# Kernel tuning notes

Measured on AMD Instinct MI355X. Metric: run time of the kernel, lower is better.

The kernel has to match this reference:

```python
import jax, jax.numpy as jnp
import numpy as np

N = 50000      # nodes
E = 600000     # edges
G = 256        # graphs in batch
HID = 128      # gcn hidden = gcn in = gcn out
EDIM = 16      # edge feature dim
EH = 64        # edge mlp hidden
NL = 4         # gcn layers
MIN_ = 200     # mol feature dim
MH = 256       # mlp hidden
MOUT = 128     # mlp out
PH = 512       # predictor hidden
PIN = HID + MOUT


def setup_inputs() -> dict:
    key = jax.random.key(0)
    ks = jax.random.split(key, 32)
    f = lambda k, s: jax.random.normal(k, s, dtype=jnp.float32)
    p = lambda k, s: 0.05 * jax.random.normal(k, s, dtype=jnp.float32)
    return {
        "x": f(ks[0], (N, HID)),
        "edge_index": jax.random.randint(ks[1], (2, E), 0, N),
        "edge_attr": f(ks[2], (E, EDIM)),
        "batch_index": jnp.sort(jax.random.randint(ks[3], (N,), 0, G)),
        "mol_features": f(ks[4], (G, MIN_)),
        # PDNConv params (stacked over NL layers)
        "conv_lin_W": p(ks[5], (NL, HID, HID)),
        "conv_mW1": p(ks[6], (NL, EDIM, EH)),
        "conv_mb1": p(ks[7], (NL, EH)),
        "conv_mW2": p(ks[8], (NL, EH)),
        "conv_mb2": p(ks[9], (NL,)),
        "conv_bias": p(ks[10], (NL, HID)),
        # dense Linear after each conv
        "gcn_W": p(ks[11], (NL, HID, HID)),
        "gcn_b": p(ks[12], (NL, HID)),
        # mol-feature MLP (n_mlp_layers=3 -> 4 linears)
        "mlp_W0": p(ks[13], (MIN_, MH)), "mlp_b0": p(ks[14], (MH,)),
        "mlp_W1": p(ks[15], (MH, MH)),   "mlp_b1": p(ks[16], (MH,)),
        "mlp_W2": p(ks[17], (MH, MH)),   "mlp_b2": p(ks[18], (MH,)),
        "mlp_W3": p(ks[19], (MH, MOUT)), "mlp_b3": p(ks[20], (MOUT,)),
        # predictor
        "pred_W0": p(ks[21], (PIN, PH)), "pred_b0": p(ks[22], (PH,)),
        "pred_W1": p(ks[23], (PH, PH)),  "pred_b1": p(ks[24], (PH,)),
        "out_W": p(ks[25], (PH, 1)),     "out_b": p(ks[26], (1,)),
    }


def _pdn_conv(h, row, col, edge_attr, lin_W, mW1, mb1, mW2, mb2, bias):
    # edge MLP -> sigmoid gate (PyG PDNConv)
    w = jax.nn.sigmoid(jnp.maximum(edge_attr @ mW1 + mb1, 0.0) @ mW2 + mb2)  # [E]
    # gcn_norm with self loops (fill weight 1.0)
    loop = jnp.arange(N)
    r = jnp.concatenate([row, loop])
    c = jnp.concatenate([col, loop])
    w_all = jnp.concatenate([w, jnp.ones((N,), h.dtype)])
    deg = jax.ops.segment_sum(w_all, c, num_segments=N)
    dinv = jnp.where(deg > 0, jax.lax.rsqrt(deg), 0.0)
    norm = dinv[r] * w_all * dinv[c]                                          # [E+N]
    hl = h @ lin_W                                                            # [N,HID]
    out = jax.ops.segment_sum(norm[:, None] * hl[r], c, num_segments=N)
    return out + bias


def reference(x, edge_index, edge_attr, batch_index, mol_features,
              conv_lin_W, conv_mW1, conv_mb1, conv_mW2, conv_mb2, conv_bias,
              gcn_W, gcn_b,
              mlp_W0, mlp_b0, mlp_W1, mlp_b1, mlp_W2, mlp_b2, mlp_W3, mlp_b3,
              pred_W0, pred_b0, pred_W1, pred_b1, out_W, out_b):
    row, col = edge_index[0], edge_index[1]
    relu = lambda v: jnp.maximum(v, 0.0)

    # GCN stack: PDNConv -> relu(Linear), x NL
    h1 = x
    for i in range(NL):
        h1 = _pdn_conv(h1, row, col, edge_attr, conv_lin_W[i], conv_mW1[i],
                       conv_mb1[i], conv_mW2[i], conv_mb2[i], conv_bias[i])
        h1 = relu(h1 @ gcn_W[i] + gcn_b[i])
    # global mean pool over graphs
    sums = jax.ops.segment_sum(h1, batch_index, num_segments=G)
    cnts = jax.ops.segment_sum(jnp.ones((N,), h1.dtype), batch_index, num_segments=G)
    h1 = sums / jnp.maximum(cnts, 1.0)[:, None]                               # [G,HID]

    # molecular-feature MLP
    h2 = relu(mol_features @ mlp_W0 + mlp_b0)
    h2 = relu(h2 @ mlp_W1 + mlp_b1)
    h2 = relu(h2 @ mlp_W2 + mlp_b2)
    h2 = relu(h2 @ mlp_W3 + mlp_b3)                                           # [G,MOUT]

    h = jnp.concatenate([h1, h2], axis=1)                                     # [G,PIN]
    h = relu(h @ pred_W0 + pred_b0)
    h = relu(h @ pred_W1 + pred_b1)
    return h @ out_W + out_b                                                  # [G,1]
```

## Files before the change

kernel.cpp:

```cpp
#include <hip/hip_runtime.h>
#include <hip/hip_bf16.h>


#define NN 50000
#define EE 600000
#define GG 256
#define HID 128
#define EDIM 16
#define EHID 64
#define NL 4
#define MIN_F 200
#define MH 256
#define MOUT 128
#define PH 512
#define PIN 256
#define SCAN_B 196
#define PCH 8

typedef __hip_bfloat16 bf16;
typedef __attribute__((ext_vector_type(8))) short bf16x8;
typedef __attribute__((ext_vector_type(4))) float f32x4;

__device__ __forceinline__ float bfl(unsigned u) { return __uint_as_float(u << 16); }
__device__ __forceinline__ float bfh(unsigned u) { return __uint_as_float(u & 0xffff0000u); }
__device__ __forceinline__ float b2f(bf16 x) { return __bfloat162float(x); }
__device__ __forceinline__ float ldf(const void* p, long i, bool bf) {
  return bf ? __bfloat162float(((const bf16*)p)[i]) : ((const float*)p)[i];
}
__device__ __forceinline__ unsigned short f2bf_bits(float v) {
  bf16 h = __float2bfloat16(v);
  return *reinterpret_cast<unsigned short*>(&h);
}

__global__ void probe_kernel(const unsigned short* __restrict__ xs, int* flag) {
  if (threadIdx.x == 0 && blockIdx.x == 0) {
    int sane = 0;
    for (int i = 0; i < 128; i++) {
      unsigned e = (xs[i] >> 7) & 0xFF;
      if (e >= 96 && e <= 159) sane++;
    }
    *flag = (sane >= 112) ? 1 : 0;
  }
}

__global__ __launch_bounds__(256) void cvt_to_bf16(const void* __restrict__ in,
                                                   unsigned short* __restrict__ outp,
                                                   int n8, const int* __restrict__ flag) {
  bool bf = *flag != 0;
  int i = blockIdx.x * 256 + threadIdx.x;
  if (i >= n8) return;
  if (bf) {
    reinterpret_cast<uint4*>(outp)[i] = reinterpret_cast<const uint4*>(in)[i];
  } else {
    const float4* p = reinterpret_cast<const float4*>(in) + (size_t)i * 2;
    float4 v0 = p[0], v1 = p[1];
    ushort4 a, b;
    a.x = f2bf_bits(v0.x); a.y = f2bf_bits(v0.y);
    a.z = f2bf_bits(v0.z); a.w = f2bf_bits(v0.w);
    b.x = f2bf_bits(v1.x); b.y = f2bf_bits(v1.y);
    b.z = f2bf_bits(v1.z); b.w = f2bf_bits(v1.w);
    reinterpret_cast<ushort4*>(outp)[i * 2] = a;
    reinterpret_cast<ushort4*>(outp)[i * 2 + 1] = b;
  }
}

__global__ __launch_bounds__(256) void cvt_molf(const void* __restrict__ in,
                                                float* __restrict__ outp,
                                                const int* __restrict__ flag) {
  bool bf = *flag != 0;
  int i = blockIdx.x * 256 + threadIdx.x;
  if (i >= GG * 50) return;
  int row = i / 50, c4 = (i % 50) * 4;
  float4 v;
  if (bf) {
    const unsigned short* p = (const unsigned short*)in + (size_t)row * MIN_F + c4;
    uint2 u = *reinterpret_cast<const uint2*>(p);
    v.x = bfl(u.x); v.y = bfh(u.x); v.z = bfl(u.y); v.w = bfh(u.y);
  } else {
    v = *reinterpret_cast<const float4*>((const float*)in + (size_t)row * MIN_F + c4);
  }
  *reinterpret_cast<float4*>(&outp[(size_t)row * 256 + c4]) = v;
}

__global__ __launch_bounds__(256) void prep_fused_w(const void* __restrict__ lin_W,
                                                    const void* __restrict__ gW,
                                                    unsigned short* __restrict__ Wt,
                                                    const int* __restrict__ flag) {
  bool bf = *flag != 0;
  int idx = blockIdx.x * 256 + threadIdx.x;
  if (idx >= 4 * 16384) return;
  int l = idx >> 14;
  int rem = idx & 16383;
  int n = rem >> 7, k = rem & 127;
  float s = 0.f;
  long lb = (long)l * 16384;
  for (int m = 0; m < 128; m++)
    s += ldf(lin_W, lb + (long)k * 128 + m, bf) * ldf(gW, lb + (long)m * 128 + n, bf);
  Wt[idx] = f2bf_bits(s);
}

__global__ __launch_bounds__(128) void prep_fused_b(const void* __restrict__ cbias,
                                                    const void* __restrict__ gW,
                                                    const void* __restrict__ gb,
                                                    float* __restrict__ bprime,
                                                    const int* __restrict__ flag) {
  bool bf = *flag != 0;
  int idx = blockIdx.x * 128 + threadIdx.x;
  if (idx >= NL * HID) return;
  int l = idx >> 7, n = idx & 127;
  float s = ldf(gb, idx, bf);
  long lb = (long)l * 16384;
  for (int k = 0; k < 128; k++)
    s += ldf(cbias, (long)l * 128 + k, bf) * ldf(gW, lb + (long)k * 128 + n, bf);
  bprime[idx] = s;
}

__global__ __launch_bounds__(256) void prep_edge_w(const void* __restrict__ mW1,
                                                   const void* __restrict__ mb1,
                                                   unsigned short* __restrict__ W1t,
                                                   const int* __restrict__ flag) {
  bool bf = *flag != 0;
  int idx = blockIdx.x * 256 + threadIdx.x;
  if (idx >= 256 * 32) return;
  int col = idx >> 5, k = idx & 31;
  float v = 0.f;
  if (k < EDIM) v = ldf(mW1, (long)(col >> 6) * (EDIM * EHID) + (long)k * EHID + (col & 63), bf);
  else if (k == EDIM) v = ldf(mb1, col, bf);
  W1t[idx] = f2bf_bits(v);
}

__global__ __launch_bounds__(256) void prep_tail(
    const void* __restrict__ mlpW0, const void* __restrict__ mlpW1,
    const void* __restrict__ mlpW2, const void* __restrict__ mlpW3,
    const void* __restrict__ predW0, const void* __restrict__ predW1,
    unsigned short* __restrict__ T, const int* __restrict__ flag) {
  bool bf = *flag != 0;
  int idx = blockIdx.x * 256 + threadIdx.x;
  const void* src; int N, Kp, Ksrc, off;
  if      (idx < 65536)  { src = mlpW0;  N = 256; Kp = 256; Ksrc = 200; off = 0; }
  else if (idx < 131072) { src = mlpW1;  N = 256; Kp = 256; Ksrc = 256; off = 65536; }
  else if (idx < 196608) { src = mlpW2;  N = 256; Kp = 256; Ksrc = 256; off = 131072; }
  else if (idx < 229376) { src = mlpW3;  N = 128; Kp = 256; Ksrc = 256; off = 196608; }
  else if (idx < 360448) { src = predW0; N = 512; Kp = 256; Ksrc = 256; off = 229376; }
  else if (idx < 622592) { src = predW1; N = 512; Kp = 512; Ksrc = 512; off = 360448; }
  else return;
  int rem = idx - off;
  int n = rem / Kp, k = rem % Kp;
  float v = (k < Ksrc) ? ldf(src, (long)k * N + n, bf) : 0.f;
  T[idx] = f2bf_bits(v);
}

__global__ __launch_bounds__(256) void count_kernel(const int* __restrict__ ei,
                                                    int* __restrict__ cnt) {
  int e = blockIdx.x * 256 + threadIdx.x;
  if (e >= EE) return;
  int c = ei[EE + e];
  c = min(max(c, 0), NN - 1);
  atomicAdd(&cnt[c], 1);
}

__global__ __launch_bounds__(256) void scan_phase1(const int* __restrict__ cnt,
                                                   int* __restrict__ bsum) {
  __shared__ int red[256];
  int tid = threadIdx.x;
  int i = blockIdx.x * 256 + tid;
  red[tid] = (i < NN) ? cnt[i] : 0;
  __syncthreads();
  for (int off = 128; off > 0; off >>= 1) {
    if (tid < off) red[tid] += red[tid + off];
    __syncthreads();
  }
  if (tid == 0) bsum[blockIdx.x] = red[0];
}

__global__ __launch_bounds__(256) void scan_phase2(int* __restrict__ bsum,
                                                   int* __restrict__ offs) {
  __shared__ int buf[256];
  int tid = threadIdx.x;
  int v = (tid < SCAN_B) ? bsum[tid] : 0;
  buf[tid] = v;
  __syncthreads();
  for (int off = 1; off < 256; off <<= 1) {
    int t = (tid >= off) ? buf[tid - off] : 0;
    __syncthreads();
    buf[tid] += t;
    __syncthreads();
  }
  if (tid < SCAN_B) bsum[tid] = buf[tid] - v;
  if (tid == 255) offs[NN] = buf[255];
}

__global__ __launch_bounds__(256) void scan_phase3(const int* __restrict__ cnt,
                                                   const int* __restrict__ bsum,
                                                   int* __restrict__ offs) {
  __shared__ int buf[256];
  int tid = threadIdx.x;
  int i = blockIdx.x * 256 + tid;
  int v = (i < NN) ? cnt[i] : 0;
  buf[tid] = v;
  __syncthreads();
  for (int off = 1; off < 256; off <<= 1) {
    int t = (tid >= off) ? buf[tid - off] : 0;
    __syncthreads();
    buf[tid] += t;
    __syncthreads();
  }
  if (i < NN) offs[i] = bsum[blockIdx.x] + buf[tid] - v;
}

__global__ __launch_bounds__(256) void fill_kernel(const int* __restrict__ ei,
                                                   const int* __restrict__ offs,
                                                   int* __restrict__ cursor,
                                                   int2* __restrict__ csr_se) {
  int e = blockIdx.x * 256 + threadIdx.x;
  if (e >= EE) return;
  int c = ei[EE + e];
  c = min(max(c, 0), NN - 1);
  int pos = offs[c] + atomicAdd(&cursor[c], 1);
  pos = min(max(pos, 0), EE - 1);
  csr_se[pos] = make_int2(ei[e], e);
}

__global__ __launch_bounds__(256) void edge_mlp_mfma(
    const void* __restrict__ eattr, const unsigned short* __restrict__ W1t,
    const void* __restrict__ mW2, const void* __restrict__ mb2,
    float* __restrict__ w_all4, const int* __restrict__ flag) {
  bool bf = *flag != 0;
  int tid = threadIdx.x;
  int wave = tid >> 6, lane = tid & 63;
  int l15 = lane & 15, quad = lane >> 4;

  bf16x8 bfrag[16];
#pragma unroll
  for (int t = 0; t < 16; t++)
    bfrag[t] = *reinterpret_cast<const bf16x8*>(&W1t[(t * 16 + l15) * 32 + quad * 8]);

  float w2v[16];
#pragma unroll
  for (int t = 0; t < 16; t++) w2v[t] = ldf(mW2, t * 16 + l15, bf);
  float b2v0 = ldf(mb2, 0, bf), b2v1 = ldf(mb2, 1, bf);
  float b2v2 = ldf(mb2, 2, bf), b2v3 = ldf(mb2, 3, bf);
  float b2 = b2v0;
  b2 = (l15 == 1) ? b2v1 : b2;
  b2 = (l15 == 2) ? b2v2 : b2;
  b2 = (l15 == 3) ? b2v3 : b2;
  bool o1 = (l15 & 1) != 0;
  bool o2 = (l15 & 2) != 0;

  int ebase = blockIdx.x * 512 + wave * 128;
#pragma unroll 1
  for (int f = 0; f < 8; f++) {
    int fbase = ebase + f * 16;
    if (fbase < EE) {
      long erow = fbase + l15;
      bf16x8 a = (bf16x8){0, 0, 0, 0, 0, 0, 0, 0};
      if (quad < 2) {
        if (bf) {
          uint4 v = *reinterpret_cast<const uint4*>((const bf16*)eattr + erow * EDIM + quad * 8);
          a = *reinterpret_cast<bf16x8*>(&v);
        } else {
          const float4* p =
              reinterpret_cast<const float4*>((const float*)eattr + erow * EDIM + quad * 8);
          float4 v0 = p[0], v1 = p[1];
          a[0] = (short)f2bf_bits(v0.x); a[1] = (short)f2bf_bits(v0.y);
          a[2] = (short)f2bf_bits(v0.z); a[3] = (short)f2bf_bits(v0.w);
          a[4] = (short)f2bf_bits(v1.x); a[5] = (short)f2bf_bits(v1.y);
          a[6] = (short)f2bf_bits(v1.z); a[7] = (short)f2bf_bits(v1.w);
        }
      }
      if (quad == 2) a[0] = (short)0x3F80;
      float s00 = 0.f, s01 = 0.f, s02 = 0.f, s03 = 0.f;
      float s10 = 0.f, s11 = 0.f, s12 = 0.f, s13 = 0.f;
      float s20 = 0.f, s21 = 0.f, s22 = 0.f, s23 = 0.f;
      float s30 = 0.f, s31 = 0.f, s32 = 0.f, s33 = 0.f;
#define DO_T(T, S0, S1, S2, S3)                                               \
  {                                                                           \
    f32x4 acc = __builtin_amdgcn_mfma_f32_16x16x32_bf16(                      \
        a, bfrag[T], (f32x4){0.f, 0.f, 0.f, 0.f}, 0, 0, 0);                   \
    S0 += fmaxf(acc.x, 0.f) * w2v[T];                                         \
    S1 += fmaxf(acc.y, 0.f) * w2v[T];                                         \
    S2 += fmaxf(acc.z, 0.f) * w2v[T];                                         \
    S3 += fmaxf(acc.w, 0.f) * w2v[T];                                         \
  }
      DO_T(0,  s00, s01, s02, s03) DO_T(1,  s00, s01, s02, s03)
      DO_T(2,  s00, s01, s02, s03) DO_T(3,  s00, s01, s02, s03)
      DO_T(4,  s10, s11, s12, s13) DO_T(5,  s10, s11, s12, s13)
      DO_T(6,  s10, s11, s12, s13) DO_T(7,  s10, s11, s12, s13)
      DO_T(8,  s20, s21, s22, s23) DO_T(9,  s20, s21, s22, s23)
      DO_T(10, s20, s21, s22, s23) DO_T(11, s20, s21, s22, s23)
      DO_T(12, s30, s31, s32, s33) DO_T(13, s30, s31, s32, s33)
      DO_T(14, s30, s31, s32, s33) DO_T(15, s30, s31, s32, s33)
#undef DO_T
#define RS_STEP1(AR, S0R, S1R) \
  float AR = (o1 ? S1R : S0R) + __shfl_xor(o1 ? S0R : S1R, 1);
      RS_STEP1(a0, s00, s10)
      RS_STEP1(a1, s01, s11)
      RS_STEP1(a2, s02, s12)
      RS_STEP1(a3, s03, s13)
      RS_STEP1(bb0, s20, s30)
      RS_STEP1(bb1, s21, s31)
      RS_STEP1(bb2, s22, s32)
      RS_STEP1(bb3, s23, s33)
#undef RS_STEP1
      float c0 = (o2 ? bb0 : a0) + __shfl_xor(o2 ? a0 : bb0, 2);
      float c1 = (o2 ? bb1 : a1) + __shfl_xor(o2 ? a1 : bb1, 2);
      float c2 = (o2 ? bb2 : a2) + __shfl_xor(o2 ? a2 : bb2, 2);
      float c3 = (o2 ? bb3 : a3) + __shfl_xor(o2 ? a3 : bb3, 2);
      c0 += __shfl_xor(c0, 4); c1 += __shfl_xor(c1, 4);
      c2 += __shfl_xor(c2, 4); c3 += __shfl_xor(c3, 4);
      c0 += __shfl_xor(c0, 8); c1 += __shfl_xor(c1, 8);
      c2 += __shfl_xor(c2, 8); c3 += __shfl_xor(c3, 8);
      if (l15 < NL) {
        float g0 = 1.f / (1.f + __expf(-(c0 + b2)));
        float g1 = 1.f / (1.f + __expf(-(c1 + b2)));
        float g2 = 1.f / (1.f + __expf(-(c2 + b2)));
        float g3 = 1.f / (1.f + __expf(-(c3 + b2)));
        w_all4[(size_t)(fbase + quad * 4 + 0) * 4 + l15] = g0;
        w_all4[(size_t)(fbase + quad * 4 + 1) * 4 + l15] = g1;
        w_all4[(size_t)(fbase + quad * 4 + 2) * 4 + l15] = g2;
        w_all4[(size_t)(fbase + quad * 4 + 3) * 4 + l15] = g3;
      }
    }
  }
}

__global__ __launch_bounds__(256) void csr_gather(const int2* __restrict__ csr_se,
                                                  const float* __restrict__ w_all4,
                                                  float* __restrict__ csr_val) {
  int k = blockIdx.x * 256 + threadIdx.x;
  if (k >= EE) return;
  int eid = csr_se[k].y;
  eid = min(max(eid, 0), EE - 1);
  float4 w = reinterpret_cast<const float4*>(w_all4)[eid];
  csr_val[k] = w.x;
  csr_val[(size_t)EE + k] = w.y;
  csr_val[2 * (size_t)EE + k] = w.z;
  csr_val[3 * (size_t)EE + k] = w.w;
}

__global__ __launch_bounds__(256) void deg_kernel(const int* __restrict__ offs,
                                                  const float* __restrict__ csr_val,
                                                  float* __restrict__ dinv4) {
  int n = blockIdx.x * 256 + threadIdx.x;
  if (n >= NN) return;
  int s = offs[n], e = offs[n + 1];
  float d0 = 1.f, d1 = 1.f, d2 = 1.f, d3 = 1.f;
  for (int k = s; k < e; k++) {
    d0 += csr_val[k];
    d1 += csr_val[EE + k];
    d2 += csr_val[2 * (size_t)EE + k];
    d3 += csr_val[3 * (size_t)EE + k];
  }
  float4 o;
  o.x = rsqrtf(d0); o.y = rsqrtf(d1); o.z = rsqrtf(d2); o.w = rsqrtf(d3);
  reinterpret_cast<float4*>(dinv4)[n] = o;
}

__global__ __launch_bounds__(256) void csr_scale_kernel(const int2* __restrict__ csr_se,
                                                        const float* __restrict__ dinv4,
                                                        float* __restrict__ csr_val) {
  int k = blockIdx.x * 256 + threadIdx.x;
  if (k >= EE) return;
  int s = csr_se[k].x;
  s = min(max(s, 0), NN - 1);
  float4 d = reinterpret_cast<const float4*>(dinv4)[s];
  csr_val[k] *= d.x;
  csr_val[(size_t)EE + k] *= d.y;
  csr_val[2 * (size_t)EE + k] *= d.z;
  csr_val[3 * (size_t)EE + k] *= d.w;
}

__global__ __launch_bounds__(256) void gemm_nodes_bf16(
    const unsigned short* __restrict__ A16, const unsigned short* __restrict__ Wt,
    const float* __restrict__ bias, unsigned short* __restrict__ out16,
    int relu) {
  __shared__ alignas(16) unsigned short sA[64 * 136];
  __shared__ alignas(16) unsigned short sW[128 * 136];
  int tid = threadIdx.x;
  int rbase = blockIdx.x * 64;

#pragma unroll
  for (int p = 0; p < 8; p++) {
    int idx8 = p * 256 + tid;
    int n = idx8 >> 4, kc = idx8 & 15;
    uint4 v = reinterpret_cast<const uint4*>(Wt)[idx8];
    *reinterpret_cast<uint4*>(&sW[n * 136 + kc * 8]) = v;
  }
#pragma unroll
  for (int p = 0; p < 4; p++) {
    int idx8 = p * 256 + tid;
    int m = idx8 >> 4, kc = idx8 & 15;
    int row = rbase + m;
    uint4 v = make_uint4(0u, 0u, 0u, 0u);
    if (row < NN)
      v = *reinterpret_cast<const uint4*>(&A16[(size_t)row * HID + kc * 8]);
    *reinterpret_cast<uint4*>(&sA[m * 136 + kc * 8]) = v;
  }
  __syncthreads();

  int wave = tid >> 6, lane = tid & 63;
  int l15 = lane & 15, quad = lane >> 4;
  int mstrip = wave * 16;

  f32x4 acc[8];
#pragma unroll
  for (int t = 0; t < 8; t++) acc[t] = (f32x4){0.f, 0.f, 0.f, 0.f};

#pragma unroll
  for (int ks = 0; ks < 4; ks++) {
    int k0 = ks * 32 + quad * 8;
    bf16x8 a = *reinterpret_cast<const bf16x8*>(&sA[(mstrip + l15) * 136 + k0]);
#pragma unroll
    for (int t = 0; t < 8; t++) {
      bf16x8 b = *reinterpret_cast<const bf16x8*>(&sW[(t * 16 + l15) * 136 + k0]);
      acc[t] = __builtin_amdgcn_mfma_f32_16x16x32_bf16(a, b, acc[t], 0, 0, 0);
    }
  }

#pragma unroll
  for (int t = 0; t < 8; t++) {
    int n = t * 16 + l15;
    float bv = bias ? bias[n] : 0.f;
#pragma unroll
    for (int r = 0; r < 4; r++) {
      int row = rbase + mstrip + quad * 4 + r;
      if (row < NN) {
        float o = acc[t][r] + bv;
        if (relu) o = fmaxf(o, 0.f);
        out16[(size_t)row * HID + n] = f2bf_bits(o);
      }
    }
  }
}

__global__ __launch_bounds__(256) void gemm_tail_mfma(
    const float* __restrict__ A, int lda, const unsigned short* __restrict__ Wt,
    int Kp, const void* __restrict__ bias, float* __restrict__ outp, int ldo,
    int relu, const int* __restrict__ flag) {
  __shared__ alignas(16) unsigned short sA[64 * 264];
  __shared__ alignas(16) unsigned short sW[64 * 264];
  int tid = threadIdx.x;
  int rbase = blockIdx.x * 64;
  int nbase = blockIdx.y * 64;
  int wave = tid >> 6, lane = tid & 63;
  int l15 = lane & 15, quad = lane >> 4;
  int mstrip = wave * 16;

  f32x4 acc[4];
#pragma unroll
  for (int t = 0; t < 4; t++) acc[t] = (f32x4){0.f, 0.f, 0.f, 0.f};

  for (int kc = 0; kc < Kp; kc += 256) {
#pragma unroll 4
    for (int p = 0; p < 16; p++) {
      int idx = p * 1024 + tid * 4;
      int m = idx >> 8, k = idx & 255;
      float4 v = *reinterpret_cast<const float4*>(&A[(size_t)(rbase + m) * lda + kc + k]);
      ushort4 b;
      b.x = f2bf_bits(v.x); b.y = f2bf_bits(v.y);
      b.z = f2bf_bits(v.z); b.w = f2bf_bits(v.w);
      *reinterpret_cast<ushort4*>(&sA[m * 264 + k]) = b;
    }
#pragma unroll 4
    for (int p = 0; p < 8; p++) {
      int idx8 = p * 256 + tid;
      int n = idx8 >> 5, kk = (idx8 & 31) * 8;
      uint4 v = *reinterpret_cast<const uint4*>(&Wt[(size_t)(nbase + n) * Kp + kc + kk]);
      *reinterpret_cast<uint4*>(&sW[n * 264 + kk]) = v;
    }
    __syncthreads();
#pragma unroll
    for (int ks = 0; ks < 8; ks++) {
      int k0 = ks * 32 + quad * 8;
      bf16x8 a = *reinterpret_cast<const bf16x8*>(&sA[(mstrip + l15) * 264 + k0]);
#pragma unroll
      for (int nt = 0; nt < 4; nt++) {
        bf16x8 b = *reinterpret_cast<const bf16x8*>(&sW[(nt * 16 + l15) * 264 + k0]);
        acc[nt] = __builtin_amdgcn_mfma_f32_16x16x32_bf16(a, b, acc[nt], 0, 0, 0);
      }
    }
    __syncthreads();
  }

  bool bf = *flag != 0;
#pragma unroll
  for (int nt = 0; nt < 4; nt++) {
    int col = nbase + nt * 16 + l15;
    float bv = ldf(bias, col, bf);
#pragma unroll
    for (int r = 0; r < 4; r++) {
      int row = rbase + mstrip + quad * 4 + r;
      float o = acc[nt][r] + bv;
      if (relu) o = fmaxf(o, 0.f);
      outp[(size_t)row * ldo + col] = o;
    }
  }
}

__global__ __launch_bounds__(128) void aggregate_kernel(
    const unsigned short* __restrict__ h16, const int* __restrict__ offs,
    const int2* __restrict__ csr_se, const float* __restrict__ csr_val,
    const float* __restrict__ dinv4, int layer,
    unsigned short* __restrict__ out16) {
  int n = blockIdx.x;
  int c = threadIdx.x;
  __shared__ int s_src[128];
  __shared__ float s_val[128];
  int start = offs[n], end = offs[n + 1];
  float acc = 0.f;
  for (int base = start; base < end; base += 128) {
    int k = base + c;
    if (k < end) {
      s_src[c] = min(max(csr_se[k].x, 0), NN - 1);
      s_val[c] = csr_val[k];
    }
    __syncthreads();
    int m = min(128, end - base);
    for (int j = 0; j < m; j++)
      acc = fmaf(s_val[j], bfl((unsigned)h16[(size_t)s_src[j] * HID + c]), acc);
    __syncthreads();
  }
  float dn = dinv4[(size_t)n * 4 + layer];
  float selfv = bfl((unsigned)h16[(size_t)n * HID + c]);
  out16[(size_t)n * HID + c] = f2bf_bits(dn * acc + dn * dn * selfv);
}

__global__ __launch_bounds__(128) void pool_partial(const unsigned short* __restrict__ h16,
                                                    const int* __restrict__ batch,
                                                    float* __restrict__ part) {
  int g = blockIdx.x, chunk = blockIdx.y, c = threadIdx.x;
  int lo = 0, hi = NN;
  while (lo < hi) { int mid = (lo + hi) >> 1; if (batch[mid] < g) lo = mid + 1; else hi = mid; }
  int start = lo;
  hi = NN;
  while (lo < hi) { int mid = (lo + hi) >> 1; if (batch[mid] < g + 1) lo = mid + 1; else hi = mid; }
  int end = lo;
  int len = end - start;
  int per = (len + PCH - 1) / PCH;
  int s = start + chunk * per;
  int e = min(s + per, end);
  float sum = 0.f;
  for (int n = s; n < e; n++) sum += bfl((unsigned)h16[(size_t)n * HID + c]);
  part[((size_t)g * PCH + chunk) * HID + c] = sum;
}

__global__ __launch_bounds__(128) void pool_combine(const float* __restrict__ part,
                                                    const int* __restrict__ batch,
                                                    float* __restrict__ cat) {
  int g = blockIdx.x, c = threadIdx.x;
  int lo = 0, hi = NN;
  while (lo < hi) { int mid = (lo + hi) >> 1; if (batch[mid] < g) lo = mid + 1; else hi = mid; }
  int start = lo;
  hi = NN;
  while (lo < hi) { int mid = (lo + hi) >> 1; if (batch[mid] < g + 1) lo = mid + 1; else hi = mid; }
  int end = lo;
  float s = 0.f;
#pragma unroll
  for (int k = 0; k < PCH; k++) s += part[((size_t)g * PCH + k) * HID + c];
  float cntf = (float)(end - start);
  cat[(size_t)g * PIN + c] = s / fmaxf(cntf, 1.f);
}

__global__ __launch_bounds__(64) void final_kernel(const float* __restrict__ A,
                                                   const void* __restrict__ W,
                                                   const void* __restrict__ b,
                                                   void* __restrict__ outp,
                                                   const int* __restrict__ flag) {
  bool bf = *flag != 0;
  int g = blockIdx.x, lane = threadIdx.x;
  float s = 0.f;
  for (int k = lane; k < PH; k += 64) s = fmaf(A[(size_t)g * PH + k], ldf(W, k, bf), s);
#pragma unroll
  for (int off = 32; off > 0; off >>= 1) s += __shfl_down(s, off);
  if (lane == 0) {
    float r = s + ldf(b, 0, bf);
    if (bf) ((bf16*)outp)[g] = __float2bfloat16(r);
    else    ((float*)outp)[g] = r;
  }
}

extern "C" void kernel_launch(void* const* d_in, const int* in_sizes, int n_in,
                              void* d_out, int out_size, void* d_ws, size_t ws_size,
                              hipStream_t stream) {
  const void* x      = d_in[0];
  const int*  ei     = (const int*)d_in[1];
  const void* eattr  = d_in[2];
  const int*  batch  = (const int*)d_in[3];
  const void* molf   = d_in[4];
  const void* lin_W  = d_in[5];
  const void* mW1    = d_in[6];
  const void* mb1    = d_in[7];
  const void* mW2    = d_in[8];
  const void* mb2    = d_in[9];
  const void* cbias  = d_in[10];
  const void* gW     = d_in[11];
  const void* gb     = d_in[12];
  const void* mlpW0  = d_in[13];
  const void* mlpb0  = d_in[14];
  const void* mlpW1  = d_in[15];
  const void* mlpb1  = d_in[16];
  const void* mlpW2  = d_in[17];
  const void* mlpb2  = d_in[18];
  const void* mlpW3  = d_in[19];
  const void* mlpb3  = d_in[20];
  const void* predW0 = d_in[21];
  const void* predb0 = d_in[22];
  const void* predW1 = d_in[23];
  const void* predb1 = d_in[24];
  const void* outW   = d_in[25];
  const void* outb   = d_in[26];

  char* base = (char*)d_ws;
  size_t off = 0;
  auto alloc = [&](size_t bytes) -> char* {
    char* p = base + off;
    off = (off + bytes + 255) & ~(size_t)255;
    return p;
  };
  unsigned short* h16  = (unsigned short*)alloc((size_t)NN * HID * 2);
  unsigned short* t16  = (unsigned short*)alloc((size_t)NN * HID * 2);
  float* dinv4    = (float*)alloc((size_t)NN * 4 * 4);
  int*   cnt      = (int*)alloc((size_t)NN * 4);
  int*   offs     = (int*)alloc((size_t)(NN + 1) * 4);
  int*   cursor   = (int*)alloc((size_t)NN * 4);
  int*   bsum     = (int*)alloc((size_t)256 * 4);
  int2*  csr_se   = (int2*)alloc((size_t)EE * 8);
  float* csr_val  = (float*)alloc((size_t)NL * EE * 4);
  float* w_all4   = (float*)alloc((size_t)EE * 4 * 4);
  unsigned short* Wt    = (unsigned short*)alloc((size_t)NL * HID * HID * 2);
  float* bprime   = (float*)alloc((size_t)NL * HID * 4);
  unsigned short* tailW = (unsigned short*)alloc((size_t)622592 * 2);
  unsigned short* edgeW = (unsigned short*)alloc((size_t)256 * 32 * 2);
  int*   flag     = (int*)alloc(256);
  float* part     = (float*)alloc((size_t)GG * PCH * HID * 4);
  float* molf32   = (float*)alloc((size_t)GG * 256 * 4);
  float* m0       = (float*)alloc((size_t)GG * MH * 4);
  float* m1       = (float*)alloc((size_t)GG * MH * 4);
  float* cat      = (float*)alloc((size_t)GG * PIN * 4);
  float* p0       = (float*)alloc((size_t)GG * PH * 4);
  float* p1       = (float*)alloc((size_t)GG * PH * 4);

  hipMemsetAsync(cnt, 0, (size_t)NN * 4, stream);
  hipMemsetAsync(cursor, 0, (size_t)NN * 4, stream);
  hipMemsetAsync(molf32, 0, (size_t)GG * 256 * 4, stream);

  probe_kernel<<<1, 64, 0, stream>>>((const unsigned short*)x, flag);

  prep_fused_w<<<256, 256, 0, stream>>>(lin_W, gW, Wt, flag);
  prep_fused_b<<<NL, 128, 0, stream>>>(cbias, gW, gb, bprime, flag);
  prep_tail<<<(622592 + 255) / 256, 256, 0, stream>>>(mlpW0, mlpW1, mlpW2, mlpW3,
                                                      predW0, predW1, tailW, flag);
  prep_edge_w<<<32, 256, 0, stream>>>(mW1, mb1, edgeW, flag);

  {
    int n8 = NN * HID / 8;
    cvt_to_bf16<<<(n8 + 255) / 256, 256, 0, stream>>>(x, h16, n8, flag);
  }
  edge_mlp_mfma<<<(EE + 511) / 512, 256, 0, stream>>>(eattr, edgeW, mW2, mb2,
                                                      w_all4, flag);
  count_kernel<<<(EE + 255) / 256, 256, 0, stream>>>(ei, cnt);
  scan_phase1<<<SCAN_B, 256, 0, stream>>>(cnt, bsum);
  scan_phase2<<<1, 256, 0, stream>>>(bsum, offs);
  scan_phase3<<<SCAN_B, 256, 0, stream>>>(cnt, bsum, offs);
  fill_kernel<<<(EE + 255) / 256, 256, 0, stream>>>(ei, offs, cursor, csr_se);
  csr_gather<<<(EE + 255) / 256, 256, 0, stream>>>(csr_se, w_all4, csr_val);
  deg_kernel<<<(NN + 255) / 256, 256, 0, stream>>>(offs, csr_val, dinv4);
  csr_scale_kernel<<<(EE + 255) / 256, 256, 0, stream>>>(csr_se, dinv4, csr_val);

  const int gemm_blocks = (NN + 63) / 64;
  for (int l = 0; l < NL; l++) {
    aggregate_kernel<<<NN, 128, 0, stream>>>(h16, offs, csr_se,
                                             csr_val + (size_t)l * EE, dinv4, l, t16);
    gemm_nodes_bf16<<<gemm_blocks, 256, 0, stream>>>(
        t16, Wt + (size_t)l * HID * HID, bprime + (size_t)l * HID, h16, 1);
  }

  pool_partial<<<dim3(GG, PCH), 128, 0, stream>>>(h16, batch, part);
  pool_combine<<<GG, 128, 0, stream>>>(part, batch, cat);

  cvt_molf<<<(GG * 50 + 255) / 256, 256, 0, stream>>>(molf, molf32, flag);
  gemm_tail_mfma<<<dim3(4, 4), 256, 0, stream>>>(molf32, 256, tailW + 0,      256, mlpb0, m0, 256, 1, flag);
  gemm_tail_mfma<<<dim3(4, 4), 256, 0, stream>>>(m0,     256, tailW + 65536,  256, mlpb1, m1, 256, 1, flag);
  gemm_tail_mfma<<<dim3(4, 4), 256, 0, stream>>>(m1,     256, tailW + 131072, 256, mlpb2, m0, 256, 1, flag);
  gemm_tail_mfma<<<dim3(4, 2), 256, 0, stream>>>(m0,     256, tailW + 196608, 256, mlpb3, cat + MOUT, 256, 1, flag);

  gemm_tail_mfma<<<dim3(4, 8), 256, 0, stream>>>(cat, 256, tailW + 229376, 256, predb0, p0, 512, 1, flag);
  gemm_tail_mfma<<<dim3(4, 8), 256, 0, stream>>>(p0,  512, tailW + 360448, 512, predb1, p1, 512, 1, flag);
  final_kernel<<<GG, 64, 0, stream>>>(p1, outW, outb, d_out, flag);
}
```

Baseline: 640.6 us.

## Vectorize SpMM aggregation with 16-byte row loads and 4-way edge split per wavefront

The per-node aggregation kernel now uses a single 64-lane wavefront instead of 128 threads. Each group of 16 lanes loads a full 256-byte bf16 feature row with uint4 loads and accumulates 8 channels per lane. Four groups process different neighbour edges in parallel, and their partial sums are combined with cross-lane shuffles. This is meant to replace many 2-byte scalar gathers with wide coalesced loads and to raise memory-level parallelism per node, at the cost of more registers and a shuffle reduction.

After: 578.7 us. 1.11x faster.

```diff
diff --git a/kernel.cpp b/kernel.cpp
--- a/kernel.cpp
+++ b/kernel.cpp
@@ -497,32 +497,62 @@
   }
 }
 
-__global__ __launch_bounds__(128) void aggregate_kernel(
+__global__ __launch_bounds__(64) void aggregate_kernel(
     const unsigned short* __restrict__ h16, const int* __restrict__ offs,
     const int2* __restrict__ csr_se, const float* __restrict__ csr_val,
     const float* __restrict__ dinv4, int layer,
     unsigned short* __restrict__ out16) {
   int n = blockIdx.x;
-  int c = threadIdx.x;
-  __shared__ int s_src[128];
-  __shared__ float s_val[128];
+  int lane = threadIdx.x;
+  int grp = lane >> 4;
+  int c16 = lane & 15;
+  __shared__ int s_src[64];
+  __shared__ float s_val[64];
   int start = offs[n], end = offs[n + 1];
-  float acc = 0.f;
-  for (int base = start; base < end; base += 128) {
-    int k = base + c;
+  float a0 = 0.f, a1 = 0.f, a2 = 0.f, a3 = 0.f;
+  float a4 = 0.f, a5 = 0.f, a6 = 0.f, a7 = 0.f;
+  for (int base = start; base < end; base += 64) {
+    int k = base + lane;
     if (k < end) {
-      s_src[c] = min(max(csr_se[k].x, 0), NN - 1);
-      s_val[c] = csr_val[k];
-    }
-    __syncthreads();
-    int m = min(128, end - base);
-    for (int j = 0; j < m; j++)
-      acc = fmaf(s_val[j], bfl((unsigned)h16[(size_t)s_src[j] * HID + c]), acc);
-    __syncthreads();
-  }
-  float dn = dinv4[(size_t)n * 4 + layer];
-  float selfv = bfl((unsigned)h16[(size_t)n * HID + c]);
-  out16[(size_t)n * HID + c] = f2bf_bits(dn * acc + dn * dn * selfv);
+      s_src[lane] = min(max(csr_se[k].x, 0), NN - 1);
+      s_val[lane] = csr_val[k];
+    }
+    __syncthreads();
+    int m = min(64, end - base);
+    for (int j = grp; j < m; j += 4) {
+      float v = s_val[j];
+      uint4 u = *reinterpret_cast<const uint4*>(&h16[(size_t)s_src[j] * HID + c16 * 8]);
+      a0 = fmaf(v, bfl(u.x), a0); a1 = fmaf(v, bfh(u.x), a1);
+      a2 = fmaf(v, bfl(u.y), a2); a3 = fmaf(v, bfh(u.y), a3);
+      a4 = fmaf(v, bfl(u.z), a4); a5 = fmaf(v, bfh(u.z), a5);
+      a6 = fmaf(v, bfl(u.w), a6); a7 = fmaf(v, bfh(u.w), a7);
+    }
+    __syncthreads();
+  }
+  a0 += __shfl_xor(a0, 16); a1 += __shfl_xor(a1, 16);
+  a2 += __shfl_xor(a2, 16); a3 += __shfl_xor(a3, 16);
+  a4 += __shfl_xor(a4, 16); a5 += __shfl_xor(a5, 16);
+  a6 += __shfl_xor(a6, 16); a7 += __shfl_xor(a7, 16);
+  a0 += __shfl_xor(a0, 32); a1 += __shfl_xor(a1, 32);
+  a2 += __shfl_xor(a2, 32); a3 += __shfl_xor(a3, 32);
+  a4 += __shfl_xor(a4, 32); a5 += __shfl_xor(a5, 32);
+  a6 += __shfl_xor(a6, 32); a7 += __shfl_xor(a7, 32);
+  if (grp == 0) {
+    float dn = dinv4[(size_t)n * 4 + layer];
+    float dn2 = dn * dn;
+    uint4 su = *reinterpret_cast<const uint4*>(&h16[(size_t)n * HID + c16 * 8]);
+    ushort4 o0, o1v;
+    o0.x  = f2bf_bits(dn * a0 + dn2 * bfl(su.x));
+    o0.y  = f2bf_bits(dn * a1 + dn2 * bfh(su.x));
+    o0.z  = f2bf_bits(dn * a2 + dn2 * bfl(su.y));
+    o0.w  = f2bf_bits(dn * a3 + dn2 * bfh(su.y));
+    o1v.x = f2bf_bits(dn * a4 + dn2 * bfl(su.z));
+    o1v.y = f2bf_bits(dn * a5 + dn2 * bfh(su.z));
+    o1v.z = f2bf_bits(dn * a6 + dn2 * bfl(su.w));
+    o1v.w = f2bf_bits(dn * a7 + dn2 * bfh(su.w));
+    *reinterpret_cast<ushort4*>(&out16[(size_t)n * HID + c16 * 8]) = o0;
+    *reinterpret_cast<ushort4*>(&out16[(size_t)n * HID + c16 * 8 + 4]) = o1v;
+  }
 }
 
 __global__ __launch_bounds__(128) void pool_partial(const unsigned short* __restrict__ h16,
@@ -669,8 +699,8 @@
 
   const int gemm_blocks = (NN + 63) / 64;
   for (int l = 0; l < NL; l++) {
-    aggregate_kernel<<<NN, 128, 0, stream>>>(h16, offs, csr_se,
-                                             csr_val + (size_t)l * EE, dinv4, l, t16);
+    aggregate_kernel<<<NN, 64, 0, stream>>>(h16, offs, csr_se,
+                                            csr_val + (size_t)l * EE, dinv4, l, t16);
     gemm_nodes_bf16<<<gemm_blocks, 256, 0, stream>>>(
         t16, Wt + (size_t)l * HID * HID, bprime + (size_t)l * HID, h16, 1);
   }
```
